# Performance work log

Hardware: AMD Instinct MI355X
Metric: run time of the kernel (lower is better)

Reference implementation:

```python
import jax, jax.numpy as jnp
import numpy as np

B, C, H, W, M = 16, 64, 256, 256, 16

def setup_inputs() -> dict:
    key = jax.random.key(0)
    ks = jax.random.split(key, 7)
    scale = 1.0 / (C * C)
    return {
        "x":   jax.random.normal(ks[0], (B, C, H, W), dtype=jnp.float32),
        "Wc":  jax.random.normal(ks[1], (C, C), dtype=jnp.float32) * (1.0 / np.sqrt(C)),
        "bc":  jax.random.normal(ks[2], (C,), dtype=jnp.float32) * 0.01,
        "w1r": jax.random.normal(ks[3], (C, C, M, M), dtype=jnp.float32) * scale,
        "w1i": jax.random.normal(ks[4], (C, C, M, M), dtype=jnp.float32) * scale,
        "w2r": jax.random.normal(ks[5], (C, C, M, M), dtype=jnp.float32) * scale,
        "w2i": jax.random.normal(ks[6], (C, C, M, M), dtype=jnp.float32) * scale,
    }

def reference(x, Wc, bc, w1r, w1i, w2r, w2i):
    b, c, h, w = x.shape
    m = w1r.shape[-1]
    # 1x1 conv residual branch: [B,C,H,W]
    res = jnp.einsum('oc,bchw->bohw', Wc, x) + bc[None, :, None, None]
    # Spectral branch: rfft2 over last two dims -> [B,C,H,W//2+1] complex64
    x_ft = jnp.fft.rfft2(x)
    w1 = w1r + 1j * w1i
    w2 = w2r + 1j * w2i
    top = jnp.einsum('bixy,ioxy->boxy', x_ft[:, :, :m, :m], w1)
    bot = jnp.einsum('bixy,ioxy->boxy', x_ft[:, :, -m:, :m], w2)
    out_ft = jnp.zeros(x_ft.shape, x_ft.dtype)
    out_ft = out_ft.at[:, :, :m, :m].set(top)
    out_ft = out_ft.at[:, :, -m:, :m].set(bot)
    spec = jnp.fft.irfft2(out_ft, s=(h, w))
    # torch F.gelu default is exact (erf) gelu
    return jax.nn.gelu(res + spec, approximate=False)
```

## Files before the change

### kernel.cpp

```cpp
#include <hip/hip_runtime.h>
#include <hip/hip_bf16.h>
#include <math.h>

#define TWO_PI_256 0.024543692606170259678f

typedef __attribute__((ext_vector_type(8))) short bf16x8;
typedef __attribute__((ext_vector_type(4))) float f32x4;

static __device__ __forceinline__ ushort bf16_rn(float a) {
    union { float f; unsigned int u; } v; v.f = a;
    unsigned int r = v.u + 0x7FFFu + ((v.u >> 16) & 1u);
    return (ushort)(r >> 16);
}
static __device__ __forceinline__ float bf16_to_f(ushort h) {
    union { unsigned int u; float f; } v; v.u = ((unsigned int)h) << 16;
    return v.f;
}
static __device__ __forceinline__ void split2(float a, ushort& hi, ushort& lo) {
    ushort h = bf16_rn(a);
    hi = h;
    lo = bf16_rn(a - bf16_to_f(h));
}

static __device__ __forceinline__ void cvt8_hi(const float* v, bf16x8& hi8) {
    union { ushort u[8]; bf16x8 v8; } H;
    #pragma unroll
    for (int j = 0; j < 8; j += 2) {
        __hip_bfloat162 hb = __float22bfloat162_rn(make_float2(v[j], v[j + 1]));
        ushort2 hu = *reinterpret_cast<ushort2*>(&hb);
        H.u[j] = hu.x; H.u[j + 1] = hu.y;
    }
    hi8 = H.v8;
}

static __device__ __forceinline__ float gelu_f(float v) {
    float z = v * fmaf(v * v, 0.10294321f, 2.3022082f);
    float e = __builtin_amdgcn_exp2f(z);
    return v - v * __builtin_amdgcn_rcpf(e + 1.0f);
}

__global__ __launch_bounds__(256) void k_prep(const float* __restrict__ Wc,
        ushort* __restrict__ Wch, ushort* __restrict__ Wcl,
        ushort* __restrict__ Tgh, ushort* __restrict__ Tgl,
        ushort* __restrict__ Tkh, ushort* __restrict__ Tkl,
        ushort* __restrict__ Th2h, ushort* __restrict__ Th2l,
        ushort* __restrict__ Th4h, ushort* __restrict__ Th4l) {
    int g = blockIdx.x * 256 + threadIdx.x;
    if (g < 4096) {
        ushort h, l; split2(Wc[g], h, l);
        Wch[g] = h; Wcl[g] = l;
    }
    int t = g - 4096;
    if (t >= 0 && t < 8192) {
        int w = t >> 5, kz = t & 31, kx = kz & 15;
        int ph = (w * kx) & 255;
        float s, c; sincosf((float)ph * TWO_PI_256, &s, &c);
        float val = (kz < 16) ? c : s;
        ushort h, l; split2(val, h, l);
        Tgh[t] = h; Tgl[t] = l;
    }
    int t2 = g - 12288;
    if (t2 >= 0 && t2 < 8192) {
        int j = t2 >> 8, w = t2 & 255, kx = j & 15;
        int ph = (w * kx) & 255;
        float s, c; sincosf((float)ph * TWO_PI_256, &s, &c);
        float val = (j < 16) ? c : s;
        ushort h, l; split2(val, h, l);
        Tkh[t2] = h; Tkl[t2] = l;
    }
    int t3 = g - 20480;
    if (t3 >= 0 && t3 < 16384) {
        int row = t3 >> 8, h = t3 & 255;
        int ky = row & 31;
        int phys = (ky < 16) ? ky : (224 + ky);
        int ph = (phys * h) & 255;
        float s, c; sincosf((float)ph * TWO_PI_256, &s, &c);
        float val = (row < 32) ? c : s;
        ushort hh, ll; split2(val, hh, ll);
        Th2h[t3] = hh; Th2l[t3] = ll;
    }
    int t4 = g - 36864;
    if (t4 >= 0 && t4 < 16384) {
        int h = t4 >> 6, col = t4 & 63;
        int ky = col & 31;
        int phys = (ky < 16) ? ky : (224 + ky);
        int ph = (phys * h) & 255;
        float s, c; sincosf((float)ph * TWO_PI_256, &s, &c);
        float val = (col < 32) ? c : s;
        ushort hh, ll; split2(val, hh, ll);
        Th4h[t4] = hh; Th4l[t4] = ll;
    }
}

__global__ __launch_bounds__(256, 3) void k_spec(const float* __restrict__ x,
        const ushort* __restrict__ Tkh, const ushort* __restrict__ Tkl,
        const ushort* __restrict__ Th2h, const ushort* __restrict__ Th2l,
        float2* __restrict__ XhT) {
    const int tid = threadIdx.x;
    const int lane = tid & 63;
    const int wv = tid >> 6;
    const int bid = blockIdx.x;
    const int bc = ((bid & 7) << 7) + (bid >> 3);
    const int l15 = lane & 15, l4 = lane >> 4;
    const int mt = wv >> 1, nt = wv & 1;

    __shared__ ushort Ah[32 * 256];
    __shared__ ushort Xwh[32 * 256];
    __shared__ float  Dl[64 * 33];

    const float* xp = x + ((size_t)bc << 16);

    const int rbase = ((mt << 4) + l15) << 8;
    const int rs = ((mt << 4) + l15) & 7;
    const int jrow = (nt << 4) + l15;

#define LDCH(pf, c) { \
    _Pragma("unroll") \
    for (int i_ = 0; i_ < 4; ++i_) { \
        int f8_ = tid + (i_ << 8); \
        int hh_ = f8_ >> 5, oct_ = f8_ & 31; \
        const float* p_ = xp + (((c) << 5) + hh_) * 256 + (oct_ << 3); \
        *(float4*)&pf[i_ * 8]     = *(const float4*)(p_); \
        *(float4*)&pf[i_ * 8 + 4] = *(const float4*)(p_ + 4); \
    } }

#define STAGE_A(pf) { \
    _Pragma("unroll") \
    for (int i_ = 0; i_ < 4; ++i_) { \
        int f8_ = tid + (i_ << 8); \
        int hh_ = f8_ >> 5, oct_ = f8_ & 31; \
        bf16x8 hi8_; \
        cvt8_hi(&pf[i_ * 8], hi8_); \
        int bx_ = oct_ ^ (hh_ & 7); \
        *(bf16x8*)(&Ah[(hh_ << 8) + (bx_ << 3)]) = hi8_; \
    } }

    float pfA[32], pfB[32];
    LDCH(pfA, 0);
    LDCH(pfB, 1);

    #pragma unroll
    for (int c = 0; c < 8; ++c) {
        __syncthreads();
        if (c & 1) { STAGE_A(pfB); } else { STAGE_A(pfA); }
        __syncthreads();
        if (c + 2 < 8) {
            if (c & 1) { LDCH(pfB, c + 2); } else { LDCH(pfA, c + 2); }
        }

        f32x4 acc = {0.f, 0.f, 0.f, 0.f};
        #pragma unroll
        for (int ks = 0; ks < 8; ++ks) {
            int boff = ((((ks << 2) + l4) ^ rs) << 3);
            bf16x8 a_h = *(const bf16x8*)(&Ah[rbase + boff]);
            int toff = (jrow << 8) + (ks << 5) + (l4 << 3);
            bf16x8 b_h = *(const bf16x8*)(Tkh + toff);
            bf16x8 b_l = *(const bf16x8*)(Tkl + toff);
            acc = __builtin_amdgcn_mfma_f32_16x16x32_bf16(a_h, b_h, acc, 0, 0, 0);
            acc = __builtin_amdgcn_mfma_f32_16x16x32_bf16(a_h, b_l, acc, 0, 0, 0);
        }
        ushort hi4[4];
        #pragma unroll
        for (int r = 0; r < 4; ++r) {
            float v = nt ? -acc[r] : acc[r];
            hi4[r] = bf16_rn(v);
        }
        int habs = (c << 5) + (mt << 4) + (l4 << 2);
        int op = (habs >> 3) ^ (jrow & 7);
        int addr = (jrow << 8) + (op << 3) + (habs & 7);
        *(ushort4*)(&Xwh[addr]) = *(ushort4*)hi4;
    }
    __syncthreads();

    f32x4 acc2[2];
    acc2[0] = (f32x4){0.f, 0.f, 0.f, 0.f};
    acc2[1] = (f32x4){0.f, 0.f, 0.f, 0.f};
    const int arow = (wv << 4) + l15;
    #pragma unroll
    for (int ks = 0; ks < 8; ++ks) {
        int aoff = (arow << 8) + (ks << 5) + (l4 << 3);
        bf16x8 a_h = *(const bf16x8*)(Th2h + aoff);
        bf16x8 a_l = *(const bf16x8*)(Th2l + aoff);
        #pragma unroll
        for (int nt2 = 0; nt2 < 2; ++nt2) {
            int col = (nt2 << 4) + l15;
            int oi = ((ks << 2) + l4) ^ (col & 7);
            bf16x8 b_h = *(const bf16x8*)(&Xwh[(col << 8) + (oi << 3)]);
            acc2[nt2] = __builtin_amdgcn_mfma_f32_16x16x32_bf16(a_h, b_h, acc2[nt2], 0, 0, 0);
            acc2[nt2] = __builtin_amdgcn_mfma_f32_16x16x32_bf16(a_l, b_h, acc2[nt2], 0, 0, 0);
        }
    }
    #pragma unroll
    for (int nt2 = 0; nt2 < 2; ++nt2)
        #pragma unroll
        for (int r = 0; r < 4; ++r)
            Dl[((wv << 4) + (l4 << 2) + r) * 33 + (nt2 << 4) + l15] = acc2[nt2][r];
    __syncthreads();

    #pragma unroll
    for (int q = 0; q < 2; ++q) {
        int m = tid + (q << 8);
        int ky = m >> 4, kx = m & 15;
        float re = Dl[ky * 33 + kx] + Dl[(32 + ky) * 33 + 16 + kx];
        float im = Dl[ky * 33 + 16 + kx] - Dl[(32 + ky) * 33 + kx];
        XhT[((size_t)m << 10) + bc] = make_float2(re, im);
    }
#undef LDCH
#undef STAGE_A
}

__global__ __launch_bounds__(256) void k_modes(const float2* __restrict__ XhT,
        const float* __restrict__ w1r, const float* __restrict__ w1i,
        const float* __restrict__ w2r, const float* __restrict__ w2i,
        float2* __restrict__ S) {
    const int tid = threadIdx.x;
    const int kyIdx = blockIdx.x >> 3;
    const int oc    = blockIdx.x & 7;
    const int xy0   = (kyIdx & 15) << 4;
    const float* __restrict__ wr = (kyIdx < 16) ? w1r : w2r;
    const float* __restrict__ wi = (kyIdx < 16) ? w1i : w2i;

    __shared__ float2 Xl[16][16][17];
    __shared__ float  Wr_l[16][8][20];
    __shared__ float  Wi_l[16][8][20];

    const int b  = tid >> 4;
    const int o8 = (tid >> 1) & 7;
    const int kh = tid & 1;

    const int s_ii = tid >> 4, s_oj = (tid >> 1) & 7, s_part = tid & 1;
    const int s_kx = tid >> 4, s_bb = tid & 15;

    float2 acc[8];
    #pragma unroll
    for (int j = 0; j < 8; ++j) acc[j] = make_float2(0.f, 0.f);

    for (int ic = 0; ic < 4; ++ic) {
        if (ic) __syncthreads();
        {
            const float* src = s_part ? wi : wr;
            size_t off = ((size_t)(((ic << 4) + s_ii) * 64 + (oc << 3) + s_oj) << 8) + xy0;
            float4 v0 = *(const float4*)(src + off);
            float4 v1 = *(const float4*)(src + off + 4);
            float4 v2 = *(const float4*)(src + off + 8);
            float4 v3 = *(const float4*)(src + off + 12);
            float* dst = s_part ? &Wi_l[s_ii][s_oj][0] : &Wr_l[s_ii][s_oj][0];
            *(float4*)(dst)      = v0;
            *(float4*)(dst + 4)  = v1;
            *(float4*)(dst + 8)  = v2;
            *(float4*)(dst + 12) = v3;
        }
        {
            const float2* src = XhT + (((size_t)((kyIdx << 4) + s_kx)) << 10)
                                    + (s_bb << 6) + (ic << 4);
            float2 xv[16];
            #pragma unroll
            for (int q = 0; q < 8; ++q)
                *(float4*)&xv[q << 1] = *(const float4*)(src + (q << 1));
            #pragma unroll
            for (int ii = 0; ii < 16; ++ii)
                Xl[s_kx][ii][s_bb] = xv[ii];
        }
        __syncthreads();

        #pragma unroll 4
        for (int ii = 0; ii < 16; ++ii) {
            float4 wr0 = *(const float4*)&Wr_l[ii][o8][kh << 3];
            float4 wr1 = *(const float4*)&Wr_l[ii][o8][(kh << 3) + 4];
            float4 wi0 = *(const float4*)&Wi_l[ii][o8][kh << 3];
            float4 wi1 = *(const float4*)&Wi_l[ii][o8][(kh << 3) + 4];
            const float wrv[8] = {wr0.x, wr0.y, wr0.z, wr0.w, wr1.x, wr1.y, wr1.z, wr1.w};
            const float wiv[8] = {wi0.x, wi0.y, wi0.z, wi0.w, wi1.x, wi1.y, wi1.z, wi1.w};
            #pragma unroll
            for (int j = 0; j < 8; ++j) {
                float2 xv = Xl[(kh << 3) + j][ii][b];
                acc[j].x = fmaf(xv.x, wrv[j], fmaf(-xv.y, wiv[j], acc[j].x));
                acc[j].y = fmaf(xv.x, wiv[j], fmaf( xv.y, wrv[j], acc[j].y));
            }
        }
    }

    const float sc = 1.52587890625e-05f;
    const int o = (oc << 3) + o8;
    float2* sp = S + (((size_t)(b << 6) + o) << 9) + (kyIdx << 4) + (kh << 3);
    #pragma unroll
    for (int q = 0; q < 4; ++q) {
        float4 v = make_float4(acc[2 * q].x * sc, acc[2 * q].y * sc,
                               acc[2 * q + 1].x * sc, acc[2 * q + 1].y * sc);
        *(float4*)(sp + (q << 1)) = v;
    }
}

static __device__ __forceinline__ void sb_put(ushort* Sbh, ushort* Sbl,
                                              int rr, int cc, float vv) {
    ushort hh, ll; split2(vv, hh, ll);
    int idx = (cc << 6) + ((((rr) >> 3) ^ (cc & 7)) << 3) + (rr & 7);
    Sbh[idx] = hh; Sbl[idx] = ll;
}

__global__ __launch_bounds__(256) void k_invh(const float2* __restrict__ S,
        const ushort* __restrict__ Th4h, const ushort* __restrict__ Th4l,
        ushort* __restrict__ Abh) {
    const int tid = threadIdx.x;
    const int lane = tid & 63;
    const int wv = tid >> 6;
    const int bid = blockIdx.x;
    const int bo = ((bid & 7) << 7) + (bid >> 3);
    const int b = bo >> 6, o = bo & 63;
    const int l15 = lane & 15, l4 = lane >> 4;

    __shared__ ushort Sbh[2048];
    __shared__ ushort Sbl[2048];
    __shared__ float  Dl[256 * 33];

    {
        float4 sv = *(const float4*)(S + ((size_t)bo << 9) + (tid << 1));
        #pragma unroll
        for (int j = 0; j < 2; ++j) {
            int m = (tid << 1) + j;
            int ky = m >> 4, kx = m & 15;
            float sr = j ? sv.z : sv.x;
            float si = j ? sv.w : sv.y;
            float scl = kx ? 2.0f : 1.0f;
            sr *= scl; si *= scl;
            sb_put(Sbh, Sbl, ky,      kx,      sr);
            sb_put(Sbh, Sbl, 32 + ky, kx,     -si);
            sb_put(Sbh, Sbl, ky,      16 + kx, -si);
            sb_put(Sbh, Sbl, 32 + ky, 16 + kx, -sr);
        }
    }
    __syncthreads();

    f32x4 acc[4][2];
    #pragma unroll
    for (int i = 0; i < 4; ++i)
        #pragma unroll
        for (int nt = 0; nt < 2; ++nt)
            acc[i][nt] = (f32x4){0.f, 0.f, 0.f, 0.f};

    #pragma unroll
    for (int i = 0; i < 4; ++i) {
        const int hrow = (((wv << 2) + i) << 4) + l15;
        #pragma unroll
        for (int ks = 0; ks < 2; ++ks) {
            int aoff = (hrow << 6) + (ks << 5) + (l4 << 3);
            bf16x8 a_h = *(const bf16x8*)(Th4h + aoff);
            bf16x8 a_l = *(const bf16x8*)(Th4l + aoff);
            #pragma unroll
            for (int nt = 0; nt < 2; ++nt) {
                int col = (nt << 4) + l15;
                int oi = ((ks << 2) + l4) ^ (col & 7);
                bf16x8 b_h = *(const bf16x8*)(&Sbh[(col << 6) + (oi << 3)]);
                bf16x8 b_l = *(const bf16x8*)(&Sbl[(col << 6) + (oi << 3)]);
                acc[i][nt] = __builtin_amdgcn_mfma_f32_16x16x32_bf16(a_h, b_h, acc[i][nt], 0, 0, 0);
                acc[i][nt] = __builtin_amdgcn_mfma_f32_16x16x32_bf16(a_h, b_l, acc[i][nt], 0, 0, 0);
                acc[i][nt] = __builtin_amdgcn_mfma_f32_16x16x32_bf16(a_l, b_h, acc[i][nt], 0, 0, 0);
            }
        }
    }
    #pragma unroll
    for (int i = 0; i < 4; ++i)
        #pragma unroll
        for (int nt = 0; nt < 2; ++nt)
            #pragma unroll
            for (int r = 0; r < 4; ++r)
                Dl[((((wv << 2) + i) << 4) + (l4 << 2) + r) * 33 + (nt << 4) + l15]
                    = acc[i][nt][r];
    __syncthreads();

    {
        const int h = tid;
        ushort hi[32];
        #pragma unroll
        for (int j = 0; j < 32; ++j)
            hi[j] = bf16_rn(Dl[h * 33 + j]);
        size_t base = (((size_t)((b << 8) + h)) << 11) + (o << 5);
        *(uint4*)(Abh + base)      = *(uint4*)&hi[0];
        *(uint4*)(Abh + base + 8)  = *(uint4*)&hi[8];
        *(uint4*)(Abh + base + 16) = *(uint4*)&hi[16];
        *(uint4*)(Abh + base + 24) = *(uint4*)&hi[24];
    }
}

__global__ __launch_bounds__(256, 3) void k_final(const float* __restrict__ x,
        const ushort* __restrict__ Wch, const ushort* __restrict__ Wcl,
        const ushort* __restrict__ Tgh, const ushort* __restrict__ Tgl,
        const ushort* __restrict__ Abh,
        const float* __restrict__ bcv, float* __restrict__ out) {
    const int tid = threadIdx.x;
    const int lane = tid & 63;
    const int wv = tid >> 6;
    const int bid = blockIdx.x;
    const int gid = ((bid >> 5) << 3) | (bid & 7);
    const int wq  = (bid >> 3) & 3;
    const int b = gid >> 6, ht = gid & 63;
    const int w0 = wq << 6;

    __shared__ ushort Xh[64][128];

    const int l15 = lane & 15, l4 = lane >> 4;
    const int mt0 = (wv >> 1) << 1;
    const int nt0 = (wv & 1) << 1;
    const int wloc = tid & 63, cb0 = tid >> 6;

    const float* xb = x + ((size_t)b << 22) + ((size_t)(ht << 2) << 8) + w0 + wloc;

    float g[2][2][8];
    #pragma unroll
    for (int i = 0; i < 2; ++i) {
        const float* xpc = xb + ((size_t)(cb0 + (i << 2)) << 19);
        #pragma unroll
        for (int j = 0; j < 8; ++j) g[0][i][j] = xpc[(size_t)j << 16];
    }

    {
        size_t gg = ((size_t)(w0 + wloc) << 5) + (cb0 << 3);
        bf16x8 th = *(const bf16x8*)(Tgh + gg);
        int bidx = (8 + cb0) ^ (wloc & 7);
        *(bf16x8*)(&Xh[0][0] + (wloc << 7) + (bidx << 3)) = th;
    }

    bf16x8 aW[2][2][2];
    #pragma unroll
    for (int mi = 0; mi < 2; ++mi) {
        int o = ((mt0 + mi) << 4) + l15;
        #pragma unroll
        for (int ks = 0; ks < 2; ++ks) {
            size_t gg = ((size_t)o << 6) + (ks << 5) + (l4 << 3);
            aW[mi][ks][0] = *(const bf16x8*)(Wch + gg);
            aW[mi][ks][1] = *(const bf16x8*)(Wcl + gg);
        }
    }
    float bias[2][4];
    #pragma unroll
    for (int mi = 0; mi < 2; ++mi)
        #pragma unroll
        for (int r = 0; r < 4; ++r)
            bias[mi][r] = bcv[((mt0 + mi) << 4) + (l4 << 2) + r];

    #pragma unroll
    for (int hh = 0; hh < 4; ++hh) {
        const int h = (ht << 2) + hh;
        const int cur = hh & 1, nxt = cur ^ 1;

        bf16x8 zH[2];
        #pragma unroll
        for (int mi = 0; mi < 2; ++mi) {
            int o = ((mt0 + mi) << 4) + l15;
            size_t gg = ((((size_t)((b << 8) + h) << 6) + o) << 5) + (l4 << 3);
            zH[mi] = *(const bf16x8*)(Abh + gg);
        }

        bf16x8 hb[2];
        cvt8_hi(g[cur][0], hb[0]);
        cvt8_hi(g[cur][1], hb[1]);

        __syncthreads();
        #pragma unroll
        for (int i = 0; i < 2; ++i) {
            int bidx = (cb0 + (i << 2)) ^ (wloc & 7);
            *(bf16x8*)(&Xh[0][0] + (wloc << 7) + (bidx << 3)) = hb[i];
        }
        __syncthreads();

        if (hh < 3) {
            #pragma unroll
            for (int i = 0; i < 2; ++i) {
                const float* xpc = xb + ((size_t)(cb0 + (i << 2)) << 19) + ((hh + 1) << 8);
                #pragma unroll
                for (int j = 0; j < 8; ++j) g[nxt][i][j] = xpc[(size_t)j << 16];
            }
        }

        f32x4 acc[2][2];
        #pragma unroll
        for (int mi = 0; mi < 2; ++mi)
            #pragma unroll
            for (int ni = 0; ni < 2; ++ni)
                acc[mi][ni] = (f32x4){0.f, 0.f, 0.f, 0.f};

        #pragma unroll
        for (int ks = 0; ks < 3; ++ks) {
            bf16x8 bh[2];
            #pragma unroll
            for (int ni = 0; ni < 2; ++ni) {
                int w = ((nt0 + ni) << 4) + l15;
                int bidx = ((ks << 2) + l4) ^ (w & 7);
                bh[ni] = *(const bf16x8*)(&Xh[0][0] + (w << 7) + (bidx << 3));
            }
            #pragma unroll
            for (int mi = 0; mi < 2; ++mi) {
                if (ks < 2) {
                    #pragma unroll
                    for (int ni = 0; ni < 2; ++ni) {
                        acc[mi][ni] = __builtin_amdgcn_mfma_f32_16x16x32_bf16(aW[mi][ks][0], bh[ni], acc[mi][ni], 0, 0, 0);
                        acc[mi][ni] = __builtin_amdgcn_mfma_f32_16x16x32_bf16(aW[mi][ks][1], bh[ni], acc[mi][ni], 0, 0, 0);
                    }
                } else {
                    #pragma unroll
                    for (int ni = 0; ni < 2; ++ni) {
                        acc[mi][ni] = __builtin_amdgcn_mfma_f32_16x16x32_bf16(zH[mi], bh[ni], acc[mi][ni], 0, 0, 0);
                    }
                }
            }
        }

        #pragma unroll
        for (int mi = 0; mi < 2; ++mi) {
            #pragma unroll
            for (int ni = 0; ni < 2; ++ni) {
                int wg = w0 + ((nt0 + ni) << 4) + l15;
                #pragma unroll
                for (int r = 0; r < 4; ++r) {
                    int o = ((mt0 + mi) << 4) + (l4 << 2) + r;
                    float v = acc[mi][ni][r] + bias[mi][r];
                    out[((size_t)((b << 6) + o) << 16) + ((size_t)h << 8) + wg] = gelu_f(v);
                }
            }
        }
    }
}

extern "C" void kernel_launch(void* const* d_in, const int* in_sizes, int n_in,
                              void* d_out, int out_size, void* d_ws, size_t ws_size,
                              hipStream_t stream) {
    const float* x   = (const float*)d_in[0];
    const float* Wc  = (const float*)d_in[1];
    const float* bcv = (const float*)d_in[2];
    const float* w1r = (const float*)d_in[3];
    const float* w1i = (const float*)d_in[4];
    const float* w2r = (const float*)d_in[5];
    const float* w2i = (const float*)d_in[6];
    float* out = (float*)d_out;

    char* wsb = (char*)d_ws;
    ushort* Abh  = (ushort*)wsb;
    float2* XhT  = (float2*)(wsb + 33554432);
    float2* S    = (float2*)(wsb + 37748736);
    ushort* Wch  = (ushort*)(wsb + 41943040);
    ushort* Wcl  = (ushort*)(wsb + 41951232);
    ushort* Tgh  = (ushort*)(wsb + 41959424);
    ushort* Tgl  = (ushort*)(wsb + 41975808);
    ushort* Tkh  = (ushort*)(wsb + 41992192);
    ushort* Tkl  = (ushort*)(wsb + 42008576);
    ushort* Th2h = (ushort*)(wsb + 42024960);
    ushort* Th2l = (ushort*)(wsb + 42057728);
    ushort* Th4h = (ushort*)(wsb + 42090496);
    ushort* Th4l = (ushort*)(wsb + 42123264);

    k_prep <<< 208, 256, 0, stream>>>(Wc, Wch, Wcl, Tgh, Tgl, Tkh, Tkl,
                                      Th2h, Th2l, Th4h, Th4l);
    k_spec <<<1024, 256, 0, stream>>>(x, Tkh, Tkl, Th2h, Th2l, XhT);
    k_modes<<< 256, 256, 0, stream>>>(XhT, w1r, w1i, w2r, w2i, S);
    k_invh <<<1024, 256, 0, stream>>>(S, Th4h, Th4l, Abh);
    k_final<<<4096, 256, 0, stream>>>(x, Wch, Wcl, Tgh, Tgl, Abh, bcv, out);
}
```

Before: 259.3 us.

## Double-buffer LDS staging in spectral and final kernels to drop a barrier

In both k_spec and k_final the shared-memory input tile is now double-buffered. The next chunk or row is converted and written into the alternate buffer after the current MFMA work, which removes one __syncthreads per loop iteration and lets the conversion overlap with other waves. k_final also prefetches the spectral Abh operand one row ahead and loads x two rows ahead. The cost is more LDS: k_spec aliases its Dl scratch onto the first A buffer but still grows overall, and k_final's tile doubles. This could limit occupancy.

```diff
diff --git a/kernel.cpp b/kernel.cpp
--- a/kernel.cpp
+++ b/kernel.cpp
@@ -104,9 +104,9 @@
     const int l15 = lane & 15, l4 = lane >> 4;
     const int mt = wv >> 1, nt = wv & 1;
 
-    __shared__ ushort Ah[32 * 256];
+    __shared__ ushort AhBuf[2][32 * 256];
     __shared__ ushort Xwh[32 * 256];
-    __shared__ float  Dl[64 * 33];
+    float* Dl = reinterpret_cast<float*>(&AhBuf[0][0]);
 
     const float* xp = x + ((size_t)bc << 16);
 
@@ -124,7 +124,7 @@
         *(float4*)&pf[i_ * 8 + 4] = *(const float4*)(p_ + 4); \
     } }
 
-#define STAGE_A(pf) { \
+#define STAGE_A(pf, dst) { \
     _Pragma("unroll") \
     for (int i_ = 0; i_ < 4; ++i_) { \
         int f8_ = tid + (i_ << 8); \
@@ -132,27 +132,27 @@
         bf16x8 hi8_; \
         cvt8_hi(&pf[i_ * 8], hi8_); \
         int bx_ = oct_ ^ (hh_ & 7); \
-        *(bf16x8*)(&Ah[(hh_ << 8) + (bx_ << 3)]) = hi8_; \
+        *(bf16x8*)(&(dst)[(hh_ << 8) + (bx_ << 3)]) = hi8_; \
     } }
 
     float pfA[32], pfB[32];
     LDCH(pfA, 0);
     LDCH(pfB, 1);
+    STAGE_A(pfA, AhBuf[0]);
 
     #pragma unroll
     for (int c = 0; c < 8; ++c) {
-        __syncthreads();
-        if (c & 1) { STAGE_A(pfB); } else { STAGE_A(pfA); }
         __syncthreads();
         if (c + 2 < 8) {
             if (c & 1) { LDCH(pfB, c + 2); } else { LDCH(pfA, c + 2); }
         }
 
+        const ushort* Acur = &AhBuf[c & 1][0];
         f32x4 acc = {0.f, 0.f, 0.f, 0.f};
         #pragma unroll
         for (int ks = 0; ks < 8; ++ks) {
             int boff = ((((ks << 2) + l4) ^ rs) << 3);
-            bf16x8 a_h = *(const bf16x8*)(&Ah[rbase + boff]);
+            bf16x8 a_h = *(const bf16x8*)(&Acur[rbase + boff]);
             int toff = (jrow << 8) + (ks << 5) + (l4 << 3);
             bf16x8 b_h = *(const bf16x8*)(Tkh + toff);
             bf16x8 b_l = *(const bf16x8*)(Tkl + toff);
@@ -169,6 +169,11 @@
         int op = (habs >> 3) ^ (jrow & 7);
         int addr = (jrow << 8) + (op << 3) + (habs & 7);
         *(ushort4*)(&Xwh[addr]) = *(ushort4*)hi4;
+
+        if (c + 1 < 8) {
+            if (c & 1) { STAGE_A(pfA, AhBuf[(c + 1) & 1]); }
+            else       { STAGE_A(pfB, AhBuf[(c + 1) & 1]); }
+        }
     }
     __syncthreads();
 
@@ -396,7 +401,7 @@
     const int b = gid >> 6, ht = gid & 63;
     const int w0 = wq << 6;
 
-    __shared__ ushort Xh[64][128];
+    __shared__ ushort Xh[2][64][128];
 
     const int l15 = lane & 15, l4 = lane >> 4;
     const int mt0 = (wv >> 1) << 1;
@@ -407,19 +412,28 @@
 
     float g[2][2][8];
     #pragma unroll
-    for (int i = 0; i < 2; ++i) {
-        const float* xpc = xb + ((size_t)(cb0 + (i << 2)) << 19);
-        #pragma unroll
-        for (int j = 0; j < 8; ++j) g[0][i][j] = xpc[(size_t)j << 16];
-    }
-
+    for (int k = 0; k < 2; ++k) {
+        #pragma unroll
+        for (int i = 0; i < 2; ++i) {
+            const float* xpc = xb + ((size_t)(cb0 + (i << 2)) << 19) + (k << 8);
+            #pragma unroll
+            for (int j = 0; j < 8; ++j) g[k][i][j] = xpc[(size_t)j << 16];
+        }
+    }
+    bf16x8 zr[2][2];
+    #pragma unroll
+    for (int mi = 0; mi < 2; ++mi) {
+        int o = ((mt0 + mi) << 4) + l15;
+        size_t gg = ((((size_t)((b << 8) + (ht << 2)) << 6) + o) << 5) + (l4 << 3);
+        zr[0][mi] = *(const bf16x8*)(Abh + gg);
+    }
     {
         size_t gg = ((size_t)(w0 + wloc) << 5) + (cb0 << 3);
         bf16x8 th = *(const bf16x8*)(Tgh + gg);
         int bidx = (8 + cb0) ^ (wloc & 7);
-        *(bf16x8*)(&Xh[0][0] + (wloc << 7) + (bidx << 3)) = th;
-    }
-
+        *(bf16x8*)(&Xh[0][0][0] + (wloc << 7) + (bidx << 3)) = th;
+        *(bf16x8*)(&Xh[1][0][0] + (wloc << 7) + (bidx << 3)) = th;
+    }
     bf16x8 aW[2][2][2];
     #pragma unroll
     for (int mi = 0; mi < 2; ++mi) {
@@ -438,37 +452,35 @@
         for (int r = 0; r < 4; ++r)
             bias[mi][r] = bcv[((mt0 + mi) << 4) + (l4 << 2) + r];
 
+    {
+        bf16x8 hb0, hb1;
+        cvt8_hi(g[0][0], hb0);
+        cvt8_hi(g[0][1], hb1);
+        int b0 = cb0 ^ (wloc & 7), b1 = (cb0 + 4) ^ (wloc & 7);
+        ushort* base = &Xh[0][0][0] + (wloc << 7);
+        *(bf16x8*)(base + (b0 << 3)) = hb0;
+        *(bf16x8*)(base + (b1 << 3)) = hb1;
+    }
+
     #pragma unroll
     for (int hh = 0; hh < 4; ++hh) {
         const int h = (ht << 2) + hh;
-        const int cur = hh & 1, nxt = cur ^ 1;
-
-        bf16x8 zH[2];
-        #pragma unroll
-        for (int mi = 0; mi < 2; ++mi) {
-            int o = ((mt0 + mi) << 4) + l15;
-            size_t gg = ((((size_t)((b << 8) + h) << 6) + o) << 5) + (l4 << 3);
-            zH[mi] = *(const bf16x8*)(Abh + gg);
-        }
-
-        bf16x8 hb[2];
-        cvt8_hi(g[cur][0], hb[0]);
-        cvt8_hi(g[cur][1], hb[1]);
 
         __syncthreads();
-        #pragma unroll
-        for (int i = 0; i < 2; ++i) {
-            int bidx = (cb0 + (i << 2)) ^ (wloc & 7);
-            *(bf16x8*)(&Xh[0][0] + (wloc << 7) + (bidx << 3)) = hb[i];
-        }
-        __syncthreads();
-
+        if (hh < 2) {
+            #pragma unroll
+            for (int i = 0; i < 2; ++i) {
+                const float* xpc = xb + ((size_t)(cb0 + (i << 2)) << 19) + ((hh + 2) << 8);
+                #pragma unroll
+                for (int j = 0; j < 8; ++j) g[hh & 1][i][j] = xpc[(size_t)j << 16];
+            }
+        }
         if (hh < 3) {
             #pragma unroll
-            for (int i = 0; i < 2; ++i) {
-                const float* xpc = xb + ((size_t)(cb0 + (i << 2)) << 19) + ((hh + 1) << 8);
-                #pragma unroll
-                for (int j = 0; j < 8; ++j) g[nxt][i][j] = xpc[(size_t)j << 16];
+            for (int mi = 0; mi < 2; ++mi) {
+                int o = ((mt0 + mi) << 4) + l15;
+                size_t gg = ((((size_t)((b << 8) + h + 1) << 6) + o) << 5) + (l4 << 3);
+                zr[(hh + 1) & 1][mi] = *(const bf16x8*)(Abh + gg);
             }
         }
 
@@ -479,6 +491,7 @@
             for (int ni = 0; ni < 2; ++ni)
                 acc[mi][ni] = (f32x4){0.f, 0.f, 0.f, 0.f};
 
+        const ushort* Xcur = &Xh[hh & 1][0][0];
         #pragma unroll
         for (int ks = 0; ks < 3; ++ks) {
             bf16x8 bh[2];
@@ -486,7 +499,7 @@
             for (int ni = 0; ni < 2; ++ni) {
                 int w = ((nt0 + ni) << 4) + l15;
                 int bidx = ((ks << 2) + l4) ^ (w & 7);
-                bh[ni] = *(const bf16x8*)(&Xh[0][0] + (w << 7) + (bidx << 3));
+                bh[ni] = *(const bf16x8*)(Xcur + (w << 7) + (bidx << 3));
             }
             #pragma unroll
             for (int mi = 0; mi < 2; ++mi) {
@@ -499,7 +512,7 @@
                 } else {
                     #pragma unroll
                     for (int ni = 0; ni < 2; ++ni) {
-                        acc[mi][ni] = __builtin_amdgcn_mfma_f32_16x16x32_bf16(zH[mi], bh[ni], acc[mi][ni], 0, 0, 0);
+                        acc[mi][ni] = __builtin_amdgcn_mfma_f32_16x16x32_bf16(zr[hh & 1][mi], bh[ni], acc[mi][ni], 0, 0, 0);
                     }
                 }
             }
@@ -517,6 +530,16 @@
                     out[((size_t)((b << 6) + o) << 16) + ((size_t)h << 8) + wg] = gelu_f(v);
                 }
             }
+        }
+
+        if (hh < 3) {
+            bf16x8 hb0, hb1;
+            cvt8_hi(g[(hh + 1) & 1][0], hb0);
+            cvt8_hi(g[(hh + 1) & 1][1], hb1);
+            int b0 = cb0 ^ (wloc & 7), b1 = (cb0 + 4) ^ (wloc & 7);
+            ushort* base = &Xh[(hh + 1) & 1][0][0] + (wloc << 7);
+            *(bf16x8*)(base + (b0 << 3)) = hb0;
+            *(bf16x8*)(base + (b1 << 3)) = hb1;
         }
     }
 }
```

New measurement: 305.8 us. 17.9% more time.
